# Performance work log

Measured on AMD Instinct MI355X. Metric: run time of the kernel, lower is better.

## Reference

```python
import jax, jax.numpy as jnp
import numpy as np

N = 50000   # nodes
E = 800000  # edges
F = 256     # in_channels
H = 256     # hidden (GCN output)


def setup_inputs() -> dict:
    key = jax.random.key(0)
    ks = jax.random.split(key, 6)
    x = jax.random.normal(ks[0], (N, F), jnp.float32)
    edge_index = jax.random.randint(ks[1], (2, E), 0, N)
    perm = jax.random.permutation(ks[2], N)
    W = jax.random.normal(ks[3], (F, H), jnp.float32) / np.sqrt(F)
    b = jnp.zeros((H,), jnp.float32)
    a = jnp.full((1,), 0.25, jnp.float32)  # PReLU slope
    disc_W = jax.random.normal(ks[4], (H, H), jnp.float32) / np.sqrt(H)
    return {"x": x, "W": W, "b": b, "a": a, "disc_W": disc_W,
            "edge_index": edge_index, "perm": perm}


def _gcn(x, W, b, src, dst, n):
    # GCNConv: linear -> symmetric-normalized aggregation (with self-loops) -> bias
    xw = x @ W  # [N, H]
    loop = jnp.arange(n)
    s = jnp.concatenate([src, loop])
    d = jnp.concatenate([dst, loop])
    ew = jnp.ones(s.shape[0], xw.dtype)
    deg = jax.ops.segment_sum(ew, d, num_segments=n)          # [N]
    dinv = jnp.where(deg > 0, jax.lax.rsqrt(deg), 0.0)
    norm = dinv[s] * dinv[d]                                   # [E+N]
    out = jax.ops.segment_sum(xw[s] * norm[:, None], d, num_segments=n)
    return out + b


def reference(x, W, b, a, disc_W, edge_index, perm):
    src, dst = edge_index[0], edge_index[1]
    n = x.shape[0]

    def encode(feat):
        h = _gcn(feat, W, b, src, dst, n)
        return jnp.where(h >= 0, h, a * h)  # PReLU

    z1 = encode(x)          # clean
    z2 = encode(x[perm])    # corrupted (row permutation)
    summary = jax.nn.sigmoid(z1.mean(axis=0))  # [H]
    wsum = disc_W @ summary                     # [H]
    pos = z1 @ wsum  # [N]
    neg = z2 @ wsum  # [N]
    return pos, neg
```

## Files before the change

kernel.cpp:

```cpp
#include <hip/hip_runtime.h>

#define N_NODES 50000
#define N_EDGES 800000
#define DIM 256
#define NB 196
#define UNROLL 8
#define MAXE (N_EDGES + N_NODES * UNROLL)
#define CSB 512
#define NCH 4
#define CCOLS 64
#define CHSZ (N_NODES * CCOLS)
#define RPB 16
#define CHB (N_NODES / RPB)

typedef __attribute__((ext_vector_type(8))) short bf16x8;
typedef __attribute__((ext_vector_type(4))) float f32x4;
typedef __attribute__((ext_vector_type(2))) float f32x2;

__device__ __forceinline__ unsigned int f2bf(float f) {
  unsigned int u = __float_as_uint(f);
  return (u + 0x7FFFu + ((u >> 16) & 1u)) >> 16;
}
__device__ __forceinline__ float bf_lo(unsigned int u) {
  return __uint_as_float(u << 16);
}
__device__ __forceinline__ float bf_hi(unsigned int u) {
  return __uint_as_float(u & 0xFFFF0000u);
}


__global__ void k_deg(const int* __restrict__ dst, int* __restrict__ deg) {
  int e = blockIdx.x * blockDim.x + threadIdx.x;
  if (e < N_EDGES) atomicAdd(&deg[dst[e]], 1);
}

__global__ __launch_bounds__(256) void k_bsum(const int* __restrict__ deg,
                                              float* __restrict__ dinv,
                                              int* __restrict__ bsum) {
  __shared__ int red[4];
  const int t = threadIdx.x;
  const int i = blockIdx.x * 256 + t;
  int pd = 0;
  if (i < N_NODES) {
    int d = deg[i];
    dinv[i] = rsqrtf((float)(d + 1));
    pd = (d + UNROLL - 1) & ~(UNROLL - 1);
  }
  int s = pd;
#pragma unroll
  for (int off = 32; off > 0; off >>= 1) s += __shfl_down(s, off);
  if ((t & 63) == 0) red[t >> 6] = s;
  __syncthreads();
  if (t == 0) bsum[blockIdx.x] = red[0] + red[1] + red[2] + red[3];
}

__global__ __launch_bounds__(256) void k_bscan(const int* __restrict__ bsum,
                                               int* __restrict__ boff,
                                               int* __restrict__ row_start) {
  __shared__ int s[256];
  const int t = threadIdx.x;
  int v = (t < NB) ? bsum[t] : 0;
  s[t] = v;
  __syncthreads();
  for (int off = 1; off < 256; off <<= 1) {
    int u = (t >= off) ? s[t - off] : 0;
    __syncthreads();
    s[t] += u;
    __syncthreads();
  }
  if (t < NB) boff[t] = s[t] - v;
  if (t == NB - 1) row_start[N_NODES] = s[NB - 1];
}

__global__ __launch_bounds__(256) void k_rowstart(const int* __restrict__ deg,
                                                  const int* __restrict__ boff,
                                                  int* __restrict__ row_start,
                                                  int* __restrict__ cursor) {
  __shared__ int s[256];
  const int t = threadIdx.x;
  const int i = blockIdx.x * 256 + t;
  int pd = (i < N_NODES) ? ((deg[i] + UNROLL - 1) & ~(UNROLL - 1)) : 0;
  s[t] = pd;
  __syncthreads();
  for (int off = 1; off < 256; off <<= 1) {
    int u = (t >= off) ? s[t - off] : 0;
    __syncthreads();
    s[t] += u;
    __syncthreads();
  }
  if (i < N_NODES) {
    int r = boff[blockIdx.x] + s[t] - pd;
    row_start[i] = r;
    cursor[i] = r;
  }
}

__global__ void k_scatter(const int* __restrict__ src, const int* __restrict__ dst,
                          const int* __restrict__ perm, const float* __restrict__ dinv,
                          int* __restrict__ cursor, uint2* __restrict__ meta) {
  int e = blockIdx.x * blockDim.x + threadIdx.x;
  if (e < N_EDGES) {
    int s = src[e], d = dst[e];
    int p = atomicAdd(&cursor[d], 1);
    meta[p] = make_uint2((unsigned)s | ((unsigned)perm[s] << 16),
                         __float_as_uint(dinv[s] * dinv[d]));
  }
}


__global__ void k_prep(const float* __restrict__ W, ushort* __restrict__ Wt) {
  int n = blockIdx.x, k = threadIdx.x;
  Wt[n * DIM + k] = (ushort)f2bf(W[k * DIM + n]);
}


__global__ __launch_bounds__(512) void k_gemm(const float* __restrict__ X,
                                              const ushort* __restrict__ Wt,
                                              ushort* __restrict__ XWC) {
  __shared__ ushort Xs[128 * 40];
  __shared__ ushort Ws[256 * 40];
  const int tid = threadIdx.x;
  const int lane = tid & 63;
  const int w = tid >> 6;
  const int wm = w >> 2, wn = w & 3;
  const int m0 = blockIdx.x * 128;
  const int l16 = lane & 15, kh = lane >> 4;

  f32x4 acc[4][4];
#pragma unroll
  for (int mf = 0; mf < 4; ++mf)
#pragma unroll
    for (int nf = 0; nf < 4; ++nf) acc[mf][nf] = (f32x4){0.f, 0.f, 0.f, 0.f};

  for (int k0 = 0; k0 < DIM; k0 += 32) {
#pragma unroll
    for (int it = 0; it < 2; ++it) {
      int idx = tid + it * 512;
      int row = idx >> 3, q = idx & 7;
      int grow = m0 + row;
      float4 v = make_float4(0.f, 0.f, 0.f, 0.f);
      if (grow < N_NODES)
        v = *reinterpret_cast<const float4*>(&X[(size_t)grow * DIM + k0 + q * 4]);
      uint2 p;
      p.x = f2bf(v.x) | (f2bf(v.y) << 16);
      p.y = f2bf(v.z) | (f2bf(v.w) << 16);
      *reinterpret_cast<uint2*>(&Xs[row * 40 + q * 4]) = p;
    }
#pragma unroll
    for (int it = 0; it < 2; ++it) {
      int idx = tid + it * 512;
      int n = idx >> 2, c = idx & 3;
      uint4 wv = *reinterpret_cast<const uint4*>(&Wt[n * DIM + k0 + c * 8]);
      *reinterpret_cast<uint4*>(&Ws[n * 40 + c * 8]) = wv;
    }
    __syncthreads();
    bf16x8 a[4], b[4];
#pragma unroll
    for (int f = 0; f < 4; ++f) {
      a[f] = *reinterpret_cast<const bf16x8*>(&Ws[(wn * 64 + f * 16 + l16) * 40 + kh * 8]);
      b[f] = *reinterpret_cast<const bf16x8*>(&Xs[(wm * 64 + f * 16 + l16) * 40 + kh * 8]);
    }
#pragma unroll
    for (int mf = 0; mf < 4; ++mf)
#pragma unroll
      for (int nf = 0; nf < 4; ++nf)
        acc[mf][nf] = __builtin_amdgcn_mfma_f32_16x16x32_bf16(a[nf], b[mf],
                                                              acc[mf][nf], 0, 0, 0);
    __syncthreads();
  }
#pragma unroll
  for (int mf = 0; mf < 4; ++mf) {
    int m = m0 + wm * 64 + mf * 16 + l16;
    if (m >= N_NODES) continue;
#pragma unroll
    for (int nf = 0; nf < 4; ++nf) {
      int nb = wn * 64 + nf * 16 + kh * 4;
      uint2 p;
      p.x = f2bf(acc[mf][nf][0]) | (f2bf(acc[mf][nf][1]) << 16);
      p.y = f2bf(acc[mf][nf][2]) | (f2bf(acc[mf][nf][3]) << 16);
      *reinterpret_cast<uint2*>(
          &XWC[(size_t)(nb >> 6) * CHSZ + (size_t)m * CCOLS + (nb & 63)]) = p;
    }
  }
}


__device__ __forceinline__ void fma8v(f32x2* A, uint4 v, f32x2 n) {
  A[0] += (f32x2){bf_lo(v.x), bf_hi(v.x)} * n;
  A[1] += (f32x2){bf_lo(v.y), bf_hi(v.y)} * n;
  A[2] += (f32x2){bf_lo(v.z), bf_hi(v.z)} * n;
  A[3] += (f32x2){bf_lo(v.w), bf_hi(v.w)} * n;
}

__global__ __launch_bounds__(256) void k_aggc(
    const ushort* __restrict__ xwc, const int* __restrict__ row_start,
    const uint2* __restrict__ meta, const int* __restrict__ perm,
    const float* __restrict__ dinv, const float* __restrict__ bias,
    const float* __restrict__ slope, ushort* __restrict__ z1,
    ushort* __restrict__ z2) {
  const int blk = blockIdx.x;
  const int ch = blk / CHB;
  const int rb = blk % CHB;
  const int tid = threadIdx.x;
  const int r = rb * RPB + (tid >> 4);
  const int l = tid & 15;
  const int eg = l >> 3;
  const int sc = l & 7;
  const ushort* xc = xwc + (size_t)ch * CHSZ;
  const unsigned scb = sc * 8;

  f32x2 a1[4] = {{0.f, 0.f}, {0.f, 0.f}, {0.f, 0.f}, {0.f, 0.f}};
  f32x2 a2[4] = {{0.f, 0.f}, {0.f, 0.f}, {0.f, 0.f}, {0.f, 0.f}};
  const int e1 = row_start[r + 1];
  for (int e = row_start[r]; e < e1; e += 8) {
    uint4 m0 = *reinterpret_cast<const uint4*>(meta + e + eg * 2);
    uint4 m1 = *reinterpret_cast<const uint4*>(meta + e + 4 + eg * 2);
    uint4 vA1 = *reinterpret_cast<const uint4*>(xc + ((m0.x & 0xFFFFu) << 6) + scb);
    uint4 vA2 = *reinterpret_cast<const uint4*>(xc + ((m0.x >> 16) << 6) + scb);
    uint4 vB1 = *reinterpret_cast<const uint4*>(xc + ((m0.z & 0xFFFFu) << 6) + scb);
    uint4 vB2 = *reinterpret_cast<const uint4*>(xc + ((m0.z >> 16) << 6) + scb);
    uint4 vC1 = *reinterpret_cast<const uint4*>(xc + ((m1.x & 0xFFFFu) << 6) + scb);
    uint4 vC2 = *reinterpret_cast<const uint4*>(xc + ((m1.x >> 16) << 6) + scb);
    uint4 vD1 = *reinterpret_cast<const uint4*>(xc + ((m1.z & 0xFFFFu) << 6) + scb);
    uint4 vD2 = *reinterpret_cast<const uint4*>(xc + ((m1.z >> 16) << 6) + scb);
    const float fA = __uint_as_float(m0.y), fB = __uint_as_float(m0.w);
    const float fC = __uint_as_float(m1.y), fD = __uint_as_float(m1.w);
    const f32x2 nA = {fA, fA}, nB = {fB, fB}, nC = {fC, fC}, nD = {fD, fD};
    fma8v(a1, vA1, nA); fma8v(a2, vA2, nA);
    fma8v(a1, vB1, nB); fma8v(a2, vB2, nB);
    fma8v(a1, vC1, nC); fma8v(a2, vC2, nC);
    fma8v(a1, vD1, nD); fma8v(a2, vD2, nD);
  }
#pragma unroll
  for (int j = 0; j < 4; ++j) {
    a1[j].x += __shfl_xor(a1[j].x, 8);
    a1[j].y += __shfl_xor(a1[j].y, 8);
    a2[j].x += __shfl_xor(a2[j].x, 8);
    a2[j].y += __shfl_xor(a2[j].y, 8);
  }
  if (eg == 0) {
    const float di = dinv[r];
    const float d2 = di * di;
    const f32x2 nd = {d2, d2};
    const int pr = perm[r];
    uint4 s1 = *reinterpret_cast<const uint4*>(xc + ((unsigned)r << 6) + scb);
    uint4 s2 = *reinterpret_cast<const uint4*>(xc + ((unsigned)pr << 6) + scb);
    fma8v(a1, s1, nd); fma8v(a2, s2, nd);
    const float* bp = bias + ch * CCOLS + sc * 8;
    float4 b0 = *reinterpret_cast<const float4*>(bp);
    float4 b1 = *reinterpret_cast<const float4*>(bp + 4);
    a1[0] += (f32x2){b0.x, b0.y}; a1[1] += (f32x2){b0.z, b0.w};
    a1[2] += (f32x2){b1.x, b1.y}; a1[3] += (f32x2){b1.z, b1.w};
    a2[0] += (f32x2){b0.x, b0.y}; a2[1] += (f32x2){b0.z, b0.w};
    a2[2] += (f32x2){b1.x, b1.y}; a2[3] += (f32x2){b1.z, b1.w};
    const float a0 = slope[0];
#pragma unroll
    for (int j = 0; j < 4; ++j) {
      a1[j].x = a1[j].x >= 0.f ? a1[j].x : a0 * a1[j].x;
      a1[j].y = a1[j].y >= 0.f ? a1[j].y : a0 * a1[j].y;
      a2[j].x = a2[j].x >= 0.f ? a2[j].x : a0 * a2[j].x;
      a2[j].y = a2[j].y >= 0.f ? a2[j].y : a0 * a2[j].y;
    }
    uint4 p1, p2;
    p1.x = f2bf(a1[0].x) | (f2bf(a1[0].y) << 16);
    p1.y = f2bf(a1[1].x) | (f2bf(a1[1].y) << 16);
    p1.z = f2bf(a1[2].x) | (f2bf(a1[2].y) << 16);
    p1.w = f2bf(a1[3].x) | (f2bf(a1[3].y) << 16);
    p2.x = f2bf(a2[0].x) | (f2bf(a2[0].y) << 16);
    p2.y = f2bf(a2[1].x) | (f2bf(a2[1].y) << 16);
    p2.z = f2bf(a2[2].x) | (f2bf(a2[2].y) << 16);
    p2.w = f2bf(a2[3].x) | (f2bf(a2[3].y) << 16);
    const size_t o = (size_t)r * DIM + ch * CCOLS + sc * 8;
    *reinterpret_cast<uint4*>(z1 + o) = p1;
    *reinterpret_cast<uint4*>(z2 + o) = p2;
  }
}


__global__ __launch_bounds__(256) void k_colsum(const ushort* __restrict__ z1,
                                                float* __restrict__ partial) {
  __shared__ float red[8 * 256];
  const int t = threadIdx.x;
  const int c8 = t & 31;
  const int g = t >> 5;
  float s[8] = {0.f, 0.f, 0.f, 0.f, 0.f, 0.f, 0.f, 0.f};
  for (int r = blockIdx.x * 8 + g; r < N_NODES; r += 8 * CSB) {
    uint4 v = *reinterpret_cast<const uint4*>(z1 + (size_t)r * DIM + c8 * 8);
    s[0] += bf_lo(v.x); s[1] += bf_hi(v.x);
    s[2] += bf_lo(v.y); s[3] += bf_hi(v.y);
    s[4] += bf_lo(v.z); s[5] += bf_hi(v.z);
    s[6] += bf_lo(v.w); s[7] += bf_hi(v.w);
  }
#pragma unroll
  for (int j = 0; j < 8; ++j) red[g * 256 + c8 * 8 + j] = s[j];
  __syncthreads();
  float tot = 0.f;
#pragma unroll
  for (int g2 = 0; g2 < 8; ++g2) tot += red[g2 * 256 + t];
  partial[blockIdx.x * 256 + t] = tot;
}

__global__ __launch_bounds__(256) void k_wsum(const float* __restrict__ partial,
                                              const float* __restrict__ disc_W,
                                              float* __restrict__ wsum) {
  __shared__ float s[DIM];
  const int t = threadIdx.x;
  float a0 = 0.f, a1 = 0.f, a2 = 0.f, a3 = 0.f;
  for (int b = 0; b < CSB; b += 4) {
    a0 += partial[(b + 0) * 256 + t];
    a1 += partial[(b + 1) * 256 + t];
    a2 += partial[(b + 2) * 256 + t];
    a3 += partial[(b + 3) * 256 + t];
  }
  float m = (a0 + a1 + a2 + a3) * (1.0f / (float)N_NODES);
  s[t] = 1.0f / (1.0f + expf(-m));
  __syncthreads();
  float acc = 0.f;
  for (int j = 0; j < DIM; j += 4) {
    float4 w4 = *reinterpret_cast<const float4*>(&disc_W[t * DIM + j]);
    acc += w4.x * s[j] + w4.y * s[j + 1] + w4.z * s[j + 2] + w4.w * s[j + 3];
  }
  wsum[t] = acc;
}


__global__ __launch_bounds__(256) void k_posneg(const ushort* __restrict__ z1,
                                                const ushort* __restrict__ z2,
                                                const float* __restrict__ wsum,
                                                float* __restrict__ pos,
                                                float* __restrict__ neg) {
  const int wid = (blockIdx.x * blockDim.x + threadIdx.x) >> 6;
  const int lane = threadIdx.x & 63;
  if (wid >= N_NODES) return;
  uint2 v1 = *reinterpret_cast<const uint2*>(z1 + (size_t)wid * DIM + lane * 4);
  uint2 v2 = *reinterpret_cast<const uint2*>(z2 + (size_t)wid * DIM + lane * 4);
  float4 w4 = *reinterpret_cast<const float4*>(&wsum[lane * 4]);
  float dp = bf_lo(v1.x) * w4.x + bf_hi(v1.x) * w4.y + bf_lo(v1.y) * w4.z + bf_hi(v1.y) * w4.w;
  float dn = bf_lo(v2.x) * w4.x + bf_hi(v2.x) * w4.y + bf_lo(v2.y) * w4.z + bf_hi(v2.y) * w4.w;
#pragma unroll
  for (int off = 32; off > 0; off >>= 1) {
    dp += __shfl_down(dp, off);
    dn += __shfl_down(dn, off);
  }
  if (lane == 0) { pos[wid] = dp; neg[wid] = dn; }
}


extern "C" void kernel_launch(void* const* d_in, const int* in_sizes, int n_in,
                              void* d_out, int out_size, void* d_ws, size_t ws_size,
                              hipStream_t stream) {
  const float* x      = (const float*)d_in[0];
  const float* W      = (const float*)d_in[1];
  const float* b      = (const float*)d_in[2];
  const float* a      = (const float*)d_in[3];
  const float* disc_W = (const float*)d_in[4];
  const int*   eidx   = (const int*)d_in[5];
  const int*   perm   = (const int*)d_in[6];
  const int* src = eidx;
  const int* dst = eidx + N_EDGES;

  constexpr size_t SZ_BFM  = (size_t)N_NODES * DIM * 2;
  constexpr size_t SZ_META = (size_t)MAXE * 8;
  constexpr size_t OFF_XWC = 0;
  constexpr size_t OFF_Z1  = OFF_XWC + SZ_BFM;
  constexpr size_t OFF_Z2  = OFF_Z1 + SZ_BFM;
  constexpr size_t OFF_WT  = OFF_Z2 + SZ_BFM;
  constexpr size_t OFF_DEG = OFF_WT + 131072;
  constexpr size_t OFF_DNV = OFF_DEG + 200192;
  constexpr size_t OFF_RS  = OFF_DNV + 200192;
  constexpr size_t OFF_CUR = OFF_RS + 200448;
  constexpr size_t OFF_MT  = OFF_CUR + 200192;
  constexpr size_t OFF_WSM = OFF_MT + SZ_META;
  constexpr size_t OFF_BS  = OFF_WSM + 1024;
  constexpr size_t OFF_BO  = OFF_BS + 1024;
  constexpr size_t OFF_PT  = OFF_BO + 1024;
  constexpr size_t NEED    = OFF_PT + (size_t)CSB * 256 * 4;
  if (ws_size < NEED) return;

  char* ws = (char*)d_ws;
  ushort* xwc    = (ushort*)(ws + OFF_XWC);
  ushort* z1     = (ushort*)(ws + OFF_Z1);
  ushort* z2     = (ushort*)(ws + OFF_Z2);
  ushort* Wt     = (ushort*)(ws + OFF_WT);
  int*    deg    = (int*)(ws + OFF_DEG);
  float*  dinv   = (float*)(ws + OFF_DNV);
  int*    rowst  = (int*)(ws + OFF_RS);
  int*    cursor = (int*)(ws + OFF_CUR);
  uint2*  meta   = (uint2*)(ws + OFF_MT);
  float*  wsum   = (float*)(ws + OFF_WSM);
  int*    bsum   = (int*)(ws + OFF_BS);
  int*    boff   = (int*)(ws + OFF_BO);
  float*  partial= (float*)(ws + OFF_PT);

  float* pos = (float*)d_out;
  float* neg = pos + N_NODES;

  hipMemsetAsync(deg, 0, N_NODES * sizeof(int), stream);
  hipMemsetAsync(meta, 0, SZ_META, stream);

  k_deg<<<(N_EDGES + 255) / 256, 256, 0, stream>>>(dst, deg);
  k_bsum<<<NB, 256, 0, stream>>>(deg, dinv, bsum);
  k_bscan<<<1, 256, 0, stream>>>(bsum, boff, rowst);
  k_rowstart<<<NB, 256, 0, stream>>>(deg, boff, rowst, cursor);
  k_scatter<<<(N_EDGES + 255) / 256, 256, 0, stream>>>(src, dst, perm, dinv,
                                                       cursor, meta);

  k_prep<<<DIM, DIM, 0, stream>>>(W, Wt);
  k_gemm<<<(N_NODES + 127) / 128, 512, 0, stream>>>(x, Wt, xwc);

  k_aggc<<<NCH * CHB, 256, 0, stream>>>(xwc, rowst, meta, perm, dinv, b, a, z1, z2);

  k_colsum<<<CSB, 256, 0, stream>>>(z1, partial);
  k_wsum<<<1, 256, 0, stream>>>(partial, disc_W, wsum);
  k_posneg<<<(N_NODES * 64 + 255) / 256, 256, 0, stream>>>(z1, z2, wsum, pos, neg);
}
```

Baseline: 236.4 us.

## Merge CSR row-offset scan kernels into one atomic-allocating kernel; shrink GEMM tile

Replaces the three-kernel degree scan (block sums, block scan, row starts) with a single kernel. Each block scans its own padded degrees and takes a base offset from a global atomic counter, so rows are no longer in node order and each row's start and end are stored as an int2 pair. This removes two launches and one serialized single-block scan. Separately, the GEMM tile drops from 128 to 64 rows with 256 threads, giving more blocks but less reuse of the W tile. The aggregation kernel also gets a small pointer-offset hoist.

```diff
diff --git a/kernel.cpp b/kernel.cpp
--- a/kernel.cpp
+++ b/kernel.cpp
@@ -34,52 +34,21 @@
   if (e < N_EDGES) atomicAdd(&deg[dst[e]], 1);
 }
 
-__global__ __launch_bounds__(256) void k_bsum(const int* __restrict__ deg,
-                                              float* __restrict__ dinv,
-                                              int* __restrict__ bsum) {
-  __shared__ int red[4];
+__global__ __launch_bounds__(256) void k_alloc(const int* __restrict__ deg,
+                                               float* __restrict__ dinv,
+                                               int* __restrict__ gcur,
+                                               int2* __restrict__ rse,
+                                               int* __restrict__ cursor) {
+  __shared__ int s[256];
+  __shared__ int base;
   const int t = threadIdx.x;
   const int i = blockIdx.x * 256 + t;
-  int pd = 0;
+  int d = 0, pd = 0;
   if (i < N_NODES) {
-    int d = deg[i];
+    d = deg[i];
     dinv[i] = rsqrtf((float)(d + 1));
     pd = (d + UNROLL - 1) & ~(UNROLL - 1);
   }
-  int s = pd;
-#pragma unroll
-  for (int off = 32; off > 0; off >>= 1) s += __shfl_down(s, off);
-  if ((t & 63) == 0) red[t >> 6] = s;
-  __syncthreads();
-  if (t == 0) bsum[blockIdx.x] = red[0] + red[1] + red[2] + red[3];
-}
-
-__global__ __launch_bounds__(256) void k_bscan(const int* __restrict__ bsum,
-                                               int* __restrict__ boff,
-                                               int* __restrict__ row_start) {
-  __shared__ int s[256];
-  const int t = threadIdx.x;
-  int v = (t < NB) ? bsum[t] : 0;
-  s[t] = v;
-  __syncthreads();
-  for (int off = 1; off < 256; off <<= 1) {
-    int u = (t >= off) ? s[t - off] : 0;
-    __syncthreads();
-    s[t] += u;
-    __syncthreads();
-  }
-  if (t < NB) boff[t] = s[t] - v;
-  if (t == NB - 1) row_start[N_NODES] = s[NB - 1];
-}
-
-__global__ __launch_bounds__(256) void k_rowstart(const int* __restrict__ deg,
-                                                  const int* __restrict__ boff,
-                                                  int* __restrict__ row_start,
-                                                  int* __restrict__ cursor) {
-  __shared__ int s[256];
-  const int t = threadIdx.x;
-  const int i = blockIdx.x * 256 + t;
-  int pd = (i < N_NODES) ? ((deg[i] + UNROLL - 1) & ~(UNROLL - 1)) : 0;
   s[t] = pd;
   __syncthreads();
   for (int off = 1; off < 256; off <<= 1) {
@@ -88,10 +57,12 @@
     s[t] += u;
     __syncthreads();
   }
+  if (t == 255) base = atomicAdd(gcur, s[255]);
+  __syncthreads();
   if (i < N_NODES) {
-    int r = boff[blockIdx.x] + s[t] - pd;
-    row_start[i] = r;
-    cursor[i] = r;
+    int rs = base + s[t] - pd;
+    rse[i] = make_int2(rs, rs + pd);
+    cursor[i] = rs;
   }
 }
 
@@ -114,16 +85,15 @@
 }
 
 
-__global__ __launch_bounds__(512) void k_gemm(const float* __restrict__ X,
+__global__ __launch_bounds__(256) void k_gemm(const float* __restrict__ X,
                                               const ushort* __restrict__ Wt,
                                               ushort* __restrict__ XWC) {
-  __shared__ ushort Xs[128 * 40];
+  __shared__ ushort Xs[64 * 40];
   __shared__ ushort Ws[256 * 40];
   const int tid = threadIdx.x;
   const int lane = tid & 63;
   const int w = tid >> 6;
-  const int wm = w >> 2, wn = w & 3;
-  const int m0 = blockIdx.x * 128;
+  const int m0 = blockIdx.x * 64;
   const int l16 = lane & 15, kh = lane >> 4;
 
   f32x4 acc[4][4];
@@ -135,7 +105,7 @@
   for (int k0 = 0; k0 < DIM; k0 += 32) {
 #pragma unroll
     for (int it = 0; it < 2; ++it) {
-      int idx = tid + it * 512;
+      int idx = tid + it * 256;
       int row = idx >> 3, q = idx & 7;
       int grow = m0 + row;
       float4 v = make_float4(0.f, 0.f, 0.f, 0.f);
@@ -147,8 +117,8 @@
       *reinterpret_cast<uint2*>(&Xs[row * 40 + q * 4]) = p;
     }
 #pragma unroll
-    for (int it = 0; it < 2; ++it) {
-      int idx = tid + it * 512;
+    for (int it = 0; it < 4; ++it) {
+      int idx = tid + it * 256;
       int n = idx >> 2, c = idx & 3;
       uint4 wv = *reinterpret_cast<const uint4*>(&Wt[n * DIM + k0 + c * 8]);
       *reinterpret_cast<uint4*>(&Ws[n * 40 + c * 8]) = wv;
@@ -157,8 +127,8 @@
     bf16x8 a[4], b[4];
 #pragma unroll
     for (int f = 0; f < 4; ++f) {
-      a[f] = *reinterpret_cast<const bf16x8*>(&Ws[(wn * 64 + f * 16 + l16) * 40 + kh * 8]);
-      b[f] = *reinterpret_cast<const bf16x8*>(&Xs[(wm * 64 + f * 16 + l16) * 40 + kh * 8]);
+      a[f] = *reinterpret_cast<const bf16x8*>(&Ws[(w * 64 + f * 16 + l16) * 40 + kh * 8]);
+      b[f] = *reinterpret_cast<const bf16x8*>(&Xs[(f * 16 + l16) * 40 + kh * 8]);
     }
 #pragma unroll
     for (int mf = 0; mf < 4; ++mf)
@@ -170,16 +140,15 @@
   }
 #pragma unroll
   for (int mf = 0; mf < 4; ++mf) {
-    int m = m0 + wm * 64 + mf * 16 + l16;
+    int m = m0 + mf * 16 + l16;
     if (m >= N_NODES) continue;
 #pragma unroll
     for (int nf = 0; nf < 4; ++nf) {
-      int nb = wn * 64 + nf * 16 + kh * 4;
+      int cb = nf * 16 + kh * 4;
       uint2 p;
       p.x = f2bf(acc[mf][nf][0]) | (f2bf(acc[mf][nf][1]) << 16);
       p.y = f2bf(acc[mf][nf][2]) | (f2bf(acc[mf][nf][3]) << 16);
-      *reinterpret_cast<uint2*>(
-          &XWC[(size_t)(nb >> 6) * CHSZ + (size_t)m * CCOLS + (nb & 63)]) = p;
+      *reinterpret_cast<uint2*>(&XWC[(size_t)w * CHSZ + (size_t)m * CCOLS + cb]) = p;
     }
   }
 }
@@ -193,7 +162,7 @@
 }
 
 __global__ __launch_bounds__(256) void k_aggc(
-    const ushort* __restrict__ xwc, const int* __restrict__ row_start,
+    const ushort* __restrict__ xwc, const int2* __restrict__ rse,
     const uint2* __restrict__ meta, const int* __restrict__ perm,
     const float* __restrict__ dinv, const float* __restrict__ bias,
     const float* __restrict__ slope, ushort* __restrict__ z1,
@@ -207,22 +176,22 @@
   const int eg = l >> 3;
   const int sc = l & 7;
   const ushort* xc = xwc + (size_t)ch * CHSZ;
-  const unsigned scb = sc * 8;
+  const ushort* xcs = xc + sc * 8;
 
   f32x2 a1[4] = {{0.f, 0.f}, {0.f, 0.f}, {0.f, 0.f}, {0.f, 0.f}};
   f32x2 a2[4] = {{0.f, 0.f}, {0.f, 0.f}, {0.f, 0.f}, {0.f, 0.f}};
-  const int e1 = row_start[r + 1];
-  for (int e = row_start[r]; e < e1; e += 8) {
+  const int2 se = rse[r];
+  for (int e = se.x; e < se.y; e += 8) {
     uint4 m0 = *reinterpret_cast<const uint4*>(meta + e + eg * 2);
     uint4 m1 = *reinterpret_cast<const uint4*>(meta + e + 4 + eg * 2);
-    uint4 vA1 = *reinterpret_cast<const uint4*>(xc + ((m0.x & 0xFFFFu) << 6) + scb);
-    uint4 vA2 = *reinterpret_cast<const uint4*>(xc + ((m0.x >> 16) << 6) + scb);
-    uint4 vB1 = *reinterpret_cast<const uint4*>(xc + ((m0.z & 0xFFFFu) << 6) + scb);
-    uint4 vB2 = *reinterpret_cast<const uint4*>(xc + ((m0.z >> 16) << 6) + scb);
-    uint4 vC1 = *reinterpret_cast<const uint4*>(xc + ((m1.x & 0xFFFFu) << 6) + scb);
-    uint4 vC2 = *reinterpret_cast<const uint4*>(xc + ((m1.x >> 16) << 6) + scb);
-    uint4 vD1 = *reinterpret_cast<const uint4*>(xc + ((m1.z & 0xFFFFu) << 6) + scb);
-    uint4 vD2 = *reinterpret_cast<const uint4*>(xc + ((m1.z >> 16) << 6) + scb);
+    uint4 vA1 = *reinterpret_cast<const uint4*>(xcs + ((m0.x & 0xFFFFu) << 6));
+    uint4 vA2 = *reinterpret_cast<const uint4*>(xcs + ((m0.x >> 16) << 6));
+    uint4 vB1 = *reinterpret_cast<const uint4*>(xcs + ((m0.z & 0xFFFFu) << 6));
+    uint4 vB2 = *reinterpret_cast<const uint4*>(xcs + ((m0.z >> 16) << 6));
+    uint4 vC1 = *reinterpret_cast<const uint4*>(xcs + ((m1.x & 0xFFFFu) << 6));
+    uint4 vC2 = *reinterpret_cast<const uint4*>(xcs + ((m1.x >> 16) << 6));
+    uint4 vD1 = *reinterpret_cast<const uint4*>(xcs + ((m1.z & 0xFFFFu) << 6));
+    uint4 vD2 = *reinterpret_cast<const uint4*>(xcs + ((m1.z >> 16) << 6));
     const float fA = __uint_as_float(m0.y), fB = __uint_as_float(m0.w);
     const float fC = __uint_as_float(m1.y), fD = __uint_as_float(m1.w);
     const f32x2 nA = {fA, fA}, nB = {fB, fB}, nC = {fC, fC}, nD = {fD, fD};
@@ -243,8 +212,8 @@
     const float d2 = di * di;
     const f32x2 nd = {d2, d2};
     const int pr = perm[r];
-    uint4 s1 = *reinterpret_cast<const uint4*>(xc + ((unsigned)r << 6) + scb);
-    uint4 s2 = *reinterpret_cast<const uint4*>(xc + ((unsigned)pr << 6) + scb);
+    uint4 s1 = *reinterpret_cast<const uint4*>(xcs + ((unsigned)r << 6));
+    uint4 s2 = *reinterpret_cast<const uint4*>(xcs + ((unsigned)pr << 6));
     fma8v(a1, s1, nd); fma8v(a2, s2, nd);
     const float* bp = bias + ch * CCOLS + sc * 8;
     float4 b0 = *reinterpret_cast<const float4*>(bp);
@@ -366,14 +335,13 @@
   constexpr size_t OFF_Z2  = OFF_Z1 + SZ_BFM;
   constexpr size_t OFF_WT  = OFF_Z2 + SZ_BFM;
   constexpr size_t OFF_DEG = OFF_WT + 131072;
+  constexpr size_t OFF_GC  = OFF_DEG + 200000;
   constexpr size_t OFF_DNV = OFF_DEG + 200192;
-  constexpr size_t OFF_RS  = OFF_DNV + 200192;
-  constexpr size_t OFF_CUR = OFF_RS + 200448;
+  constexpr size_t OFF_RSE = OFF_DNV + 200192;
+  constexpr size_t OFF_CUR = OFF_RSE + 400128;
   constexpr size_t OFF_MT  = OFF_CUR + 200192;
   constexpr size_t OFF_WSM = OFF_MT + SZ_META;
-  constexpr size_t OFF_BS  = OFF_WSM + 1024;
-  constexpr size_t OFF_BO  = OFF_BS + 1024;
-  constexpr size_t OFF_PT  = OFF_BO + 1024;
+  constexpr size_t OFF_PT  = OFF_WSM + 1024;
   constexpr size_t NEED    = OFF_PT + (size_t)CSB * 256 * 4;
   if (ws_size < NEED) return;
 
@@ -383,32 +351,29 @@
   ushort* z2     = (ushort*)(ws + OFF_Z2);
   ushort* Wt     = (ushort*)(ws + OFF_WT);
   int*    deg    = (int*)(ws + OFF_DEG);
+  int*    gcur   = (int*)(ws + OFF_GC);
   float*  dinv   = (float*)(ws + OFF_DNV);
-  int*    rowst  = (int*)(ws + OFF_RS);
+  int2*   rse    = (int2*)(ws + OFF_RSE);
   int*    cursor = (int*)(ws + OFF_CUR);
   uint2*  meta   = (uint2*)(ws + OFF_MT);
   float*  wsum   = (float*)(ws + OFF_WSM);
-  int*    bsum   = (int*)(ws + OFF_BS);
-  int*    boff   = (int*)(ws + OFF_BO);
   float*  partial= (float*)(ws + OFF_PT);
 
   float* pos = (float*)d_out;
   float* neg = pos + N_NODES;
 
-  hipMemsetAsync(deg, 0, N_NODES * sizeof(int), stream);
+  hipMemsetAsync(deg, 0, 200064, stream);
   hipMemsetAsync(meta, 0, SZ_META, stream);
 
   k_deg<<<(N_EDGES + 255) / 256, 256, 0, stream>>>(dst, deg);
-  k_bsum<<<NB, 256, 0, stream>>>(deg, dinv, bsum);
-  k_bscan<<<1, 256, 0, stream>>>(bsum, boff, rowst);
-  k_rowstart<<<NB, 256, 0, stream>>>(deg, boff, rowst, cursor);
+  k_alloc<<<NB, 256, 0, stream>>>(deg, dinv, gcur, rse, cursor);
   k_scatter<<<(N_EDGES + 255) / 256, 256, 0, stream>>>(src, dst, perm, dinv,
                                                        cursor, meta);
 
   k_prep<<<DIM, DIM, 0, stream>>>(W, Wt);
-  k_gemm<<<(N_NODES + 127) / 128, 512, 0, stream>>>(x, Wt, xwc);
-
-  k_aggc<<<NCH * CHB, 256, 0, stream>>>(xwc, rowst, meta, perm, dinv, b, a, z1, z2);
+  k_gemm<<<(N_NODES + 63) / 64, 256, 0, stream>>>(x, Wt, xwc);
+
+  k_aggc<<<NCH * CHB, 256, 0, stream>>>(xwc, rse, meta, perm, dinv, b, a, z1, z2);
 
   k_colsum<<<CSB, 256, 0, stream>>>(z1, partial);
   k_wsum<<<1, 256, 0, stream>>>(partial, disc_W, wsum);
```

Measured after the change: 240.2 us. About the same (+1.6%).
